# Optimization experiments

Hardware: AMD Instinct MI355X
Metric: run time of the kernel (lower is better)

## Reference

```python
import jax, jax.numpy as jnp
import numpy as np

LN_EPS = 1e-5  # torch nn.LayerNorm default
L2_EPS = 1e-12  # F.normalize default


def layer_norm(x, gamma, beta):
    mu = jnp.mean(x, axis=-1, keepdims=True)
    var = jnp.mean(jnp.square(x - mu), axis=-1, keepdims=True)
    return (x - mu) * jax.lax.rsqrt(var + LN_EPS) * gamma + beta


def l2_normalize(x):
    n = jnp.linalg.norm(x, axis=-1, keepdims=True)
    return x / jnp.maximum(n, L2_EPS)


def setup_inputs() -> dict:
    key = jax.random.key(0)
    k_x, k_mu = jax.random.split(key, 2)
    B, C, H, W = 4, 512, 128, 128
    K, M = 19, 5  # num_classes, num_components_per_class
    x = jax.random.normal(k_x, (B, C, H, W), dtype=jnp.float32)
    means = 0.02 * jax.random.normal(k_mu, (K, M, C), dtype=jnp.float32)  # trunc_normal_(std=0.02)
    diagonal = jnp.ones((K, M, C), dtype=jnp.float32)
    feat_gamma = jnp.ones((C,), dtype=jnp.float32)
    feat_beta = jnp.zeros((C,), dtype=jnp.float32)
    mask_gamma = jnp.ones((K,), dtype=jnp.float32)
    mask_beta = jnp.zeros((K,), dtype=jnp.float32)
    return dict(x=x, means=means, diagonal=diagonal,
                feat_gamma=feat_gamma, feat_beta=feat_beta,
                mask_gamma=mask_gamma, mask_beta=mask_beta)


def reference(x, means, diagonal, feat_gamma, feat_beta, mask_gamma, mask_beta):
    B, C, H, W = x.shape
    K, M, D = means.shape
    # rearrange 'b c h w -> (b h w) c'
    f = jnp.transpose(x, (0, 2, 3, 1)).reshape(-1, C)  # (N, D)
    f = layer_norm(f, feat_gamma, feat_beta)
    f = l2_normalize(f)
    # means are re-normalized in-place each forward
    mu = l2_normalize(means).reshape(K * M, D)          # (P, D), P = K*M
    sigma = diagonal.reshape(K * M, D)                  # diagonal scale (std)
    inv_var = 1.0 / jnp.square(sigma)
    # Mahalanobis distance via quadratic expansion (avoids (N,P,D) intermediate):
    # sum_d ((f - mu)/sigma)^2 = f^2 . iv - 2 f . (mu*iv) + sum(mu^2 * iv)
    q1 = jnp.square(f) @ inv_var.T                      # (N, P)
    q2 = f @ (mu * inv_var).T                           # (N, P)
    q3 = jnp.sum(jnp.square(mu) * inv_var, axis=-1)     # (P,)
    maha = q1 - 2.0 * q2 + q3[None, :]
    log_det = jnp.sum(jnp.log(sigma), axis=-1)          # sum log sigma, (P,)
    half_log2pi = 0.5 * D * jnp.log(2.0 * jnp.pi)
    log_prob = -0.5 * maha - log_det[None, :] - half_log2pi  # (N, P)
    log_prob = log_prob.reshape(-1, K, M)
    m_prob = jnp.max(log_prob, axis=-1)                 # amax over components, (N, K)
    out = layer_norm(m_prob, mask_gamma, mask_beta)
    # rearrange '(b h w) k -> b k h w'
    out_seg = jnp.transpose(out.reshape(B, H, W, K), (0, 3, 1, 2))
    return out_seg
```

## Files before the change

kernel.cpp:

```cpp
#include <hip/hip_runtime.h>
#include <math.h>

#define C_ 512
#define HW_ 16384
#define K_ 19
#define M_ 5
#define P_ 95
#define P2 96
#define TPX 32
#define NBLK 2048
#define HL2PI 470.49652900081467f

typedef __attribute__((ext_vector_type(8))) short short8;
typedef __attribute__((ext_vector_type(4))) float float4v;

static __device__ __forceinline__ short f2bf(float f) {
  unsigned u = __builtin_bit_cast(unsigned, f);
  unsigned r = (u + 0x7fffu + ((u >> 16) & 1u)) >> 16;
  return (short)r;
}

__device__ __forceinline__ float block_reduce_sum(float v, volatile float* red) {
#pragma unroll
  for (int o = 32; o; o >>= 1) v += __shfl_down(v, o);
  const int lane = threadIdx.x & 63, wv = threadIdx.x >> 6;
  if (lane == 0) red[wv] = v;
  __syncthreads();
  float r = red[0] + red[1] + red[2] + red[3];
  __syncthreads();
  return r;
}

__global__ __launch_bounds__(256) void prep_kernel(
    const float* __restrict__ means, const float* __restrict__ diag,
    short* __restrict__ wbf, float* __restrict__ cterm) {
  const int p = blockIdx.x;
  const int tid = threadIdx.x;
  __shared__ float red[4];
  if (p >= P_) {
    for (int c = tid; c < C_; c += 256) {
      wbf[p * 1024 + c] = 0;
      wbf[p * 1024 + 512 + c] = 0;
    }
    if (tid == 0) cterm[p] = 0.f;
    return;
  }
  const float* mrow = means + (size_t)p * C_;
  const float* srow = diag + (size_t)p * C_;
  float m0 = mrow[tid], m1 = mrow[tid + 256];
  float ss = block_reduce_sum(m0 * m0 + m1 * m1, red);
  float rden = 1.f / fmaxf(sqrtf(ss), 1e-12f);
  float q3 = 0.f, ld = 0.f;
#pragma unroll
  for (int t = 0; t < 2; t++) {
    int c = tid + t * 256;
    float m = mrow[c], s = srow[c];
    float mu = m * rden;
    float iv = 1.f / (s * s);
    wbf[p * 1024 + c] = f2bf(iv);
    wbf[p * 1024 + 512 + c] = f2bf(mu * iv);
    q3 += mu * mu * iv;
    ld += logf(s);
  }
  q3 = block_reduce_sum(q3, red);
  ld = block_reduce_sum(ld, red);
  if (tid == 0) cterm[p] = -0.5f * q3 - ld - HL2PI;
}

__global__ __launch_bounds__(256) void main_kernel(
    const float* __restrict__ x,
    const float* __restrict__ fg, const float* __restrict__ fb,
    const float* __restrict__ mg, const float* __restrict__ mb,
    const short* __restrict__ wbf, const float* __restrict__ cterm,
    float* __restrict__ out) {
  __shared__ __align__(16) char raw[65536];
  __shared__ float red0[8 * TPX], red1[8 * TPX];
  __shared__ float meanA[TPX], rstdA[TPX], rnA[TPX], rn2A[TPX];
  __shared__ float mean2A[TPX], rstd2A[TPX];
  __shared__ float mpr[TPX * 20];

  const int tid = threadIdx.x;
  const int px = tid & 31, part = tid >> 5;
  const int n0 = blockIdx.x * TPX;
  const int b = n0 >> 14;
  const int rem = n0 & 16383;
  const int h = rem >> 7;
  const int w0 = rem & 127;

  const float* xp = x + (size_t)b * C_ * HW_ + h * 128 + w0 + px;
  const int cbase = part * 64;
  float xr[64];
#pragma unroll
  for (int i = 0; i < 64; i++) xr[i] = xp[(size_t)(cbase + i) * HW_];
  {
    float s = 0.f, q = 0.f;
#pragma unroll
    for (int i = 0; i < 64; i++) {
      s += xr[i];
      q += xr[i] * xr[i];
    }
    red0[part * 32 + px] = s;
    red1[part * 32 + px] = q;
  }
  __syncthreads();
  if (tid < 32) {
    float ss = 0.f, qq = 0.f;
#pragma unroll
    for (int i = 0; i < 8; i++) {
      ss += red0[i * 32 + tid];
      qq += red1[i * 32 + tid];
    }
    float mean = ss * (1.f / C_);
    float var = qq * (1.f / C_) - mean * mean;
    meanA[tid] = mean;
    rstdA[tid] = rsqrtf(var + 1e-5f);
  }
  __syncthreads();

  {
    const float mean = meanA[px], rstd = rstdA[px];
    float s2 = 0.f;
    const int t_ = px >> 4;
    const int lq = px & 15;
#pragma unroll
    for (int t8 = 0; t8 < 8; t8++) {
      const int c0 = cbase + t8 * 8;
      short8 v2p, vp;
#pragma unroll
      for (int j = 0; j < 8; j++) {
        const int c = c0 + j;
        float v = (xr[t8 * 8 + j] - mean) * rstd;
        v = fmaf(v, fg[c], fb[c]);
        s2 += v * v;
        v2p[j] = f2bf(v * v);
        vp[j] = f2bf(v);
      }
      const int l = (((c0 >> 3) & 3) << 4) | lq;
      const int ks1 = c0 >> 5;
      const int ks2 = 16 + ks1;
      *(short8*)(raw + (((t_ * 32 + ks1) << 10) | (l << 4))) = v2p;
      *(short8*)(raw + (((t_ * 32 + ks2) << 10) | (l << 4))) = vp;
    }
    red0[part * 32 + px] = s2;
  }
  __syncthreads();
  if (tid < 32) {
    float ss = 0.f;
#pragma unroll
    for (int i = 0; i < 8; i++) ss += red0[i * 32 + tid];
    float rn = 1.f / fmaxf(sqrtf(ss), 1e-12f);
    rnA[tid] = rn;
    rn2A[tid] = rn * rn;
  }
  __syncthreads();

  const int wv = tid >> 6, lane = tid & 63;
  const int pbase = (wv & 1) * 3;
  const int khalf = wv >> 1;
  const int lm = lane & 15, lk = lane >> 4;
  float4v acc[3][2] = {};
  const short* wrow = wbf + (((pbase * 16 + lm) << 10) | (khalf << 9) | (lk << 3));
#pragma unroll 4
  for (int ksl = 0; ksl < 16; ksl++) {
    const int ks = khalf * 16 + ksl;
    short8 a0 = *(const short8*)(wrow + ksl * 32);
    short8 a1 = *(const short8*)(wrow + 16384 + ksl * 32);
    short8 a2 = *(const short8*)(wrow + 32768 + ksl * 32);
    short8 b0 = *(const short8*)(raw + ((ks << 10) | (lane << 4)));
    short8 b1 = *(const short8*)(raw + (((32 + ks) << 10) | (lane << 4)));
    acc[0][0] = __builtin_amdgcn_mfma_f32_16x16x32_bf16(a0, b0, acc[0][0], 0, 0, 0);
    acc[0][1] = __builtin_amdgcn_mfma_f32_16x16x32_bf16(a0, b1, acc[0][1], 0, 0, 0);
    acc[1][0] = __builtin_amdgcn_mfma_f32_16x16x32_bf16(a1, b0, acc[1][0], 0, 0, 0);
    acc[1][1] = __builtin_amdgcn_mfma_f32_16x16x32_bf16(a1, b1, acc[1][1], 0, 0, 0);
    acc[2][0] = __builtin_amdgcn_mfma_f32_16x16x32_bf16(a2, b0, acc[2][0], 0, 0, 0);
    acc[2][1] = __builtin_amdgcn_mfma_f32_16x16x32_bf16(a2, b1, acc[2][1], 0, 0, 0);
  }
  __syncthreads();
  float* lp = (float*)raw;

  if (khalf == 0) {
#pragma unroll
    for (int i = 0; i < 3; i++) {
      const int prow = (pbase + i) * 16 + lk * 4;
#pragma unroll
      for (int r = 0; r < 4; r++) {
        const float ct = cterm[prow + r];
#pragma unroll
        for (int t = 0; t < 2; t++) {
          const int pxx = t * 16 + lm;
          lp[pxx * 100 + prow + r] = fmaf(-0.5f * rn2A[pxx], acc[i][t][r], ct);
        }
      }
    }
  }
  __syncthreads();
  if (khalf == 1) {
#pragma unroll
    for (int i = 0; i < 3; i++) {
      const int prow = (pbase + i) * 16 + lk * 4;
#pragma unroll
      for (int r = 0; r < 4; r++) {
#pragma unroll
        for (int t = 0; t < 2; t++) {
          const int pxx = t * 16 + lm;
          lp[pxx * 100 + prow + r] += rnA[pxx] * acc[i][t][r];
        }
      }
    }
  }
  __syncthreads();

  for (int idx = tid; idx < TPX * K_; idx += 256) {
    const int pxx = idx / K_;
    const int k = idx - pxx * K_;
    const float* row = lp + pxx * 100 + k * M_;
    float mv = row[0];
#pragma unroll
    for (int m = 1; m < M_; m++) mv = fmaxf(mv, row[m]);
    mpr[pxx * 20 + k] = mv;
  }
  __syncthreads();
  if (tid < 32) {
    float ss = 0.f;
    for (int k = 0; k < K_; k++) ss += mpr[tid * 20 + k];
    float m2 = ss * (1.f / K_);
    float qq = 0.f;
    for (int k = 0; k < K_; k++) {
      float d = mpr[tid * 20 + k] - m2;
      qq += d * d;
    }
    mean2A[tid] = m2;
    rstd2A[tid] = rsqrtf(qq * (1.f / K_) + 1e-5f);
  }
  __syncthreads();
  float* obase = out + ((size_t)(b * K_) * 128 + h) * 128 + w0;
  for (int idx = tid; idx < TPX * K_; idx += 256) {
    const int k = idx >> 5, pxx = idx & 31;
    float v = fmaf((mpr[pxx * 20 + k] - mean2A[pxx]) * rstd2A[pxx], mg[k], mb[k]);
    obase[(size_t)k * HW_ + pxx] = v;
  }
}

extern "C" void kernel_launch(void* const* d_in, const int* in_sizes, int n_in,
                              void* d_out, int out_size, void* d_ws, size_t ws_size,
                              hipStream_t stream) {
  const float* x = (const float*)d_in[0];
  const float* means = (const float*)d_in[1];
  const float* diag = (const float*)d_in[2];
  const float* fg = (const float*)d_in[3];
  const float* fb = (const float*)d_in[4];
  const float* mg = (const float*)d_in[5];
  const float* mb = (const float*)d_in[6];
  float* out = (float*)d_out;

  short* wbf = (short*)d_ws;
  float* cterm = (float*)((char*)d_ws + (size_t)P2 * 1024 * 2);

  prep_kernel<<<P2, 256, 0, stream>>>(means, diag, wbf, cterm);
  main_kernel<<<NBLK, 256, 0, stream>>>(x, fg, fb, mg, mb, wbf, cterm, out);
}
```

Measured before the change: 81.45 us.

## Halve pixels per block, swizzle LDS layout, split partial-sum buffers

```diff
diff --git a/kernel.cpp b/kernel.cpp
--- a/kernel.cpp
+++ b/kernel.cpp
@@ -7,8 +7,8 @@
 #define M_ 5
 #define P_ 95
 #define P2 96
-#define TPX 32
-#define NBLK 2048
+#define TPX 16
+#define NBLK 4096
 #define HL2PI 470.49652900081467f
 
 typedef __attribute__((ext_vector_type(8))) short short8;
@@ -73,14 +73,16 @@
     const float* __restrict__ mg, const float* __restrict__ mb,
     const short* __restrict__ wbf, const float* __restrict__ cterm,
     float* __restrict__ out) {
-  __shared__ __align__(16) char raw[65536];
-  __shared__ float red0[8 * TPX], red1[8 * TPX];
+  __shared__ __align__(16) char raw[32768];
+  __shared__ float red0[4 * TPX], red1[4 * TPX];
   __shared__ float meanA[TPX], rstdA[TPX], rnA[TPX], rn2A[TPX];
   __shared__ float mean2A[TPX], rstd2A[TPX];
   __shared__ float mpr[TPX * 20];
 
   const int tid = threadIdx.x;
-  const int px = tid & 31, part = tid >> 5;
+  const int px = tid & 15;
+  const int part = tid >> 4;
+  const int wv = tid >> 6, lane = tid & 63;
   const int n0 = blockIdx.x * TPX;
   const int b = n0 >> 14;
   const int rem = n0 & 16383;
@@ -88,28 +90,26 @@
   const int w0 = rem & 127;
 
   const float* xp = x + (size_t)b * C_ * HW_ + h * 128 + w0 + px;
-  const int cbase = part * 64;
-  float xr[64];
-#pragma unroll
-  for (int i = 0; i < 64; i++) xr[i] = xp[(size_t)(cbase + i) * HW_];
+  const int cbase = part * 32;
+  float xr[32];
+#pragma unroll
+  for (int i = 0; i < 32; i++) xr[i] = xp[(size_t)(cbase + i) * HW_];
   {
     float s = 0.f, q = 0.f;
 #pragma unroll
-    for (int i = 0; i < 64; i++) {
+    for (int i = 0; i < 32; i++) {
       s += xr[i];
       q += xr[i] * xr[i];
     }
-    red0[part * 32 + px] = s;
-    red1[part * 32 + px] = q;
-  }
-  __syncthreads();
-  if (tid < 32) {
+    s += __shfl_xor(s, 16); s += __shfl_xor(s, 32);
+    q += __shfl_xor(q, 16); q += __shfl_xor(q, 32);
+    if (lane < 16) { red0[wv * 16 + px] = s; red1[wv * 16 + px] = q; }
+  }
+  __syncthreads();
+  if (tid < 16) {
     float ss = 0.f, qq = 0.f;
 #pragma unroll
-    for (int i = 0; i < 8; i++) {
-      ss += red0[i * 32 + tid];
-      qq += red1[i * 32 + tid];
-    }
+    for (int i = 0; i < 4; i++) { ss += red0[i * 16 + tid]; qq += red1[i * 16 + tid]; }
     float mean = ss * (1.f / C_);
     float var = qq * (1.f / C_) - mean * mean;
     meanA[tid] = mean;
@@ -120,10 +120,9 @@
   {
     const float mean = meanA[px], rstd = rstdA[px];
     float s2 = 0.f;
-    const int t_ = px >> 4;
-    const int lq = px & 15;
-#pragma unroll
-    for (int t8 = 0; t8 < 8; t8++) {
+    const int swz = (part & 3) << 8;
+#pragma unroll
+    for (int t8 = 0; t8 < 4; t8++) {
       const int c0 = cbase + t8 * 8;
       short8 v2p, vp;
 #pragma unroll
@@ -135,77 +134,59 @@
         v2p[j] = f2bf(v * v);
         vp[j] = f2bf(v);
       }
-      const int l = (((c0 >> 3) & 3) << 4) | lq;
-      const int ks1 = c0 >> 5;
-      const int ks2 = 16 + ks1;
-      *(short8*)(raw + (((t_ * 32 + ks1) << 10) | (l << 4))) = v2p;
-      *(short8*)(raw + (((t_ * 32 + ks2) << 10) | (l << 4))) = vp;
-    }
-    red0[part * 32 + px] = s2;
-  }
-  __syncthreads();
-  if (tid < 32) {
+      const int a1 = ((part << 10) | (t8 << 8) | (px << 4)) ^ swz;
+      *(short8*)(raw + a1) = v2p;
+      *(short8*)(raw + a1 + 16384) = vp;
+    }
+    s2 += __shfl_xor(s2, 16); s2 += __shfl_xor(s2, 32);
+    if (lane < 16) red0[wv * 16 + px] = s2;
+  }
+  __syncthreads();
+  if (tid < 16) {
     float ss = 0.f;
 #pragma unroll
-    for (int i = 0; i < 8; i++) ss += red0[i * 32 + tid];
+    for (int i = 0; i < 4; i++) ss += red0[i * 16 + tid];
     float rn = 1.f / fmaxf(sqrtf(ss), 1e-12f);
     rnA[tid] = rn;
     rn2A[tid] = rn * rn;
   }
   __syncthreads();
 
-  const int wv = tid >> 6, lane = tid & 63;
   const int pbase = (wv & 1) * 3;
   const int khalf = wv >> 1;
   const int lm = lane & 15, lk = lane >> 4;
-  float4v acc[3][2] = {};
-  const short* wrow = wbf + (((pbase * 16 + lm) << 10) | (khalf << 9) | (lk << 3));
+  float4v acc[3] = {};
+  const short* wrow = wbf + (((pbase * 16 + lm) << 10) + (khalf << 9) + (lk << 3));
 #pragma unroll 4
   for (int ksl = 0; ksl < 16; ksl++) {
     const int ks = khalf * 16 + ksl;
     short8 a0 = *(const short8*)(wrow + ksl * 32);
     short8 a1 = *(const short8*)(wrow + 16384 + ksl * 32);
     short8 a2 = *(const short8*)(wrow + 32768 + ksl * 32);
-    short8 b0 = *(const short8*)(raw + ((ks << 10) | (lane << 4)));
-    short8 b1 = *(const short8*)(raw + (((32 + ks) << 10) | (lane << 4)));
-    acc[0][0] = __builtin_amdgcn_mfma_f32_16x16x32_bf16(a0, b0, acc[0][0], 0, 0, 0);
-    acc[0][1] = __builtin_amdgcn_mfma_f32_16x16x32_bf16(a0, b1, acc[0][1], 0, 0, 0);
-    acc[1][0] = __builtin_amdgcn_mfma_f32_16x16x32_bf16(a1, b0, acc[1][0], 0, 0, 0);
-    acc[1][1] = __builtin_amdgcn_mfma_f32_16x16x32_bf16(a1, b1, acc[1][1], 0, 0, 0);
-    acc[2][0] = __builtin_amdgcn_mfma_f32_16x16x32_bf16(a2, b0, acc[2][0], 0, 0, 0);
-    acc[2][1] = __builtin_amdgcn_mfma_f32_16x16x32_bf16(a2, b1, acc[2][1], 0, 0, 0);
-  }
-  __syncthreads();
-  float* lp = (float*)raw;
+    short8 bf = *(const short8*)(raw + (((ks << 10) | (lane << 4)) ^ ((ks & 3) << 8)));
+    acc[0] = __builtin_amdgcn_mfma_f32_16x16x32_bf16(a0, bf, acc[0], 0, 0, 0);
+    acc[1] = __builtin_amdgcn_mfma_f32_16x16x32_bf16(a1, bf, acc[1], 0, 0, 0);
+    acc[2] = __builtin_amdgcn_mfma_f32_16x16x32_bf16(a2, bf, acc[2], 0, 0, 0);
+  }
+  __syncthreads();
+  float* lp1 = (float*)raw;
+  float* lp2 = (float*)(raw + 8192);
 
   if (khalf == 0) {
 #pragma unroll
     for (int i = 0; i < 3; i++) {
       const int prow = (pbase + i) * 16 + lk * 4;
 #pragma unroll
-      for (int r = 0; r < 4; r++) {
-        const float ct = cterm[prow + r];
-#pragma unroll
-        for (int t = 0; t < 2; t++) {
-          const int pxx = t * 16 + lm;
-          lp[pxx * 100 + prow + r] = fmaf(-0.5f * rn2A[pxx], acc[i][t][r], ct);
-        }
-      }
-    }
-  }
-  __syncthreads();
-  if (khalf == 1) {
+      for (int r = 0; r < 4; r++)
+        lp1[lm * 96 + prow + r] = fmaf(-0.5f * rn2A[lm], acc[i][r], cterm[prow + r]);
+    }
+  } else {
 #pragma unroll
     for (int i = 0; i < 3; i++) {
       const int prow = (pbase + i) * 16 + lk * 4;
 #pragma unroll
-      for (int r = 0; r < 4; r++) {
-#pragma unroll
-        for (int t = 0; t < 2; t++) {
-          const int pxx = t * 16 + lm;
-          lp[pxx * 100 + prow + r] += rnA[pxx] * acc[i][t][r];
-        }
-      }
+      for (int r = 0; r < 4; r++)
+        lp2[lm * 96 + prow + r] = rnA[lm] * acc[i][r];
     }
   }
   __syncthreads();
@@ -213,14 +194,15 @@
   for (int idx = tid; idx < TPX * K_; idx += 256) {
     const int pxx = idx / K_;
     const int k = idx - pxx * K_;
-    const float* row = lp + pxx * 100 + k * M_;
-    float mv = row[0];
-#pragma unroll
-    for (int m = 1; m < M_; m++) mv = fmaxf(mv, row[m]);
+    const float* r1 = lp1 + pxx * 96 + k * M_;
+    const float* r2 = lp2 + pxx * 96 + k * M_;
+    float mv = r1[0] + r2[0];
+#pragma unroll
+    for (int m = 1; m < M_; m++) mv = fmaxf(mv, r1[m] + r2[m]);
     mpr[pxx * 20 + k] = mv;
   }
   __syncthreads();
-  if (tid < 32) {
+  if (tid < 16) {
     float ss = 0.f;
     for (int k = 0; k < K_; k++) ss += mpr[tid * 20 + k];
     float m2 = ss * (1.f / K_);
@@ -235,7 +217,7 @@
   __syncthreads();
   float* obase = out + ((size_t)(b * K_) * 128 + h) * 128 + w0;
   for (int idx = tid; idx < TPX * K_; idx += 256) {
-    const int k = idx >> 5, pxx = idx & 31;
+    const int k = idx >> 4, pxx = idx & 15;
     float v = fmaf((mpr[pxx * 20 + k] - mean2A[pxx]) * rstd2A[pxx], mg[k], mb[k]);
     obase[(size_t)k * HW_ + pxx] = v;
   }
```

Measured after the change: 126.2 us. +55.0%, slower.

## Make main kernel persistent with 4 tiles per block and prefetch next tile's input

Applied to the files above, without the earlier changes.

```diff
diff --git a/kernel.cpp b/kernel.cpp
--- a/kernel.cpp
+++ b/kernel.cpp
@@ -8,7 +8,8 @@
 #define P_ 95
 #define P2 96
 #define TPX 32
-#define NBLK 2048
+#define GRID_ 512
+#define TILES_ 4
 #define HL2PI 470.49652900081467f
 
 typedef __attribute__((ext_vector_type(8))) short short8;
@@ -78,166 +79,188 @@
   __shared__ float meanA[TPX], rstdA[TPX], rnA[TPX], rn2A[TPX];
   __shared__ float mean2A[TPX], rstd2A[TPX];
   __shared__ float mpr[TPX * 20];
+  __shared__ float fgs[C_], fbs[C_], cts[P2], mgs[K_ + 1], mbs[K_ + 1];
 
   const int tid = threadIdx.x;
   const int px = tid & 31, part = tid >> 5;
-  const int n0 = blockIdx.x * TPX;
-  const int b = n0 >> 14;
-  const int rem = n0 & 16383;
-  const int h = rem >> 7;
-  const int w0 = rem & 127;
-
-  const float* xp = x + (size_t)b * C_ * HW_ + h * 128 + w0 + px;
-  const int cbase = part * 64;
-  float xr[64];
-#pragma unroll
-  for (int i = 0; i < 64; i++) xr[i] = xp[(size_t)(cbase + i) * HW_];
-  {
-    float s = 0.f, q = 0.f;
-#pragma unroll
-    for (int i = 0; i < 64; i++) {
-      s += xr[i];
-      q += xr[i] * xr[i];
-    }
-    red0[part * 32 + px] = s;
-    red1[part * 32 + px] = q;
-  }
-  __syncthreads();
-  if (tid < 32) {
-    float ss = 0.f, qq = 0.f;
-#pragma unroll
-    for (int i = 0; i < 8; i++) {
-      ss += red0[i * 32 + tid];
-      qq += red1[i * 32 + tid];
-    }
-    float mean = ss * (1.f / C_);
-    float var = qq * (1.f / C_) - mean * mean;
-    meanA[tid] = mean;
-    rstdA[tid] = rsqrtf(var + 1e-5f);
-  }
-  __syncthreads();
-
-  {
-    const float mean = meanA[px], rstd = rstdA[px];
-    float s2 = 0.f;
-    const int t_ = px >> 4;
-    const int lq = px & 15;
-#pragma unroll
-    for (int t8 = 0; t8 < 8; t8++) {
-      const int c0 = cbase + t8 * 8;
-      short8 v2p, vp;
-#pragma unroll
-      for (int j = 0; j < 8; j++) {
-        const int c = c0 + j;
-        float v = (xr[t8 * 8 + j] - mean) * rstd;
-        v = fmaf(v, fg[c], fb[c]);
-        s2 += v * v;
-        v2p[j] = f2bf(v * v);
-        vp[j] = f2bf(v);
-      }
-      const int l = (((c0 >> 3) & 3) << 4) | lq;
-      const int ks1 = c0 >> 5;
-      const int ks2 = 16 + ks1;
-      *(short8*)(raw + (((t_ * 32 + ks1) << 10) | (l << 4))) = v2p;
-      *(short8*)(raw + (((t_ * 32 + ks2) << 10) | (l << 4))) = vp;
-    }
-    red0[part * 32 + px] = s2;
-  }
-  __syncthreads();
-  if (tid < 32) {
-    float ss = 0.f;
-#pragma unroll
-    for (int i = 0; i < 8; i++) ss += red0[i * 32 + tid];
-    float rn = 1.f / fmaxf(sqrtf(ss), 1e-12f);
-    rnA[tid] = rn;
-    rn2A[tid] = rn * rn;
-  }
-  __syncthreads();
-
   const int wv = tid >> 6, lane = tid & 63;
   const int pbase = (wv & 1) * 3;
   const int khalf = wv >> 1;
   const int lm = lane & 15, lk = lane >> 4;
-  float4v acc[3][2] = {};
-  const short* wrow = wbf + (((pbase * 16 + lm) << 10) | (khalf << 9) | (lk << 3));
+  const int cbase = part * 64;
+
+  for (int i = tid; i < C_; i += 256) { fgs[i] = fg[i]; fbs[i] = fb[i]; }
+  if (tid < P2) cts[tid] = cterm[tid];
+  if (tid < K_) { mgs[tid] = mg[tid]; mbs[tid] = mb[tid]; }
+
+  float xr[64];
+  {
+    const int n0 = blockIdx.x * TPX;
+    const int b = n0 >> 14, rem = n0 & 16383, h = rem >> 7, w0 = rem & 127;
+    const float* xp = x + (size_t)b * C_ * HW_ + h * 128 + w0 + px;
+#pragma unroll
+    for (int i = 0; i < 64; i++) xr[i] = xp[(size_t)(cbase + i) * HW_];
+  }
+
+  for (int t = 0; t < TILES_; ++t) {
+    const int n0 = (blockIdx.x + GRID_ * t) * TPX;
+    const int b = n0 >> 14, rem = n0 & 16383, h = rem >> 7, w0 = rem & 127;
+
+    {
+      float s = 0.f, q = 0.f;
+#pragma unroll
+      for (int i = 0; i < 64; i++) {
+        s += xr[i];
+        q += xr[i] * xr[i];
+      }
+      red0[part * 32 + px] = s;
+      red1[part * 32 + px] = q;
+    }
+    __syncthreads();
+    if (tid < 32) {
+      float ss = 0.f, qq = 0.f;
+#pragma unroll
+      for (int i = 0; i < 8; i++) {
+        ss += red0[i * 32 + tid];
+        qq += red1[i * 32 + tid];
+      }
+      float mean = ss * (1.f / C_);
+      float var = qq * (1.f / C_) - mean * mean;
+      meanA[tid] = mean;
+      rstdA[tid] = rsqrtf(var + 1e-5f);
+    }
+    __syncthreads();
+
+    {
+      const float mean = meanA[px], rstd = rstdA[px];
+      float s2 = 0.f;
+      const int t_ = px >> 4;
+      const int lq = px & 15;
+#pragma unroll
+      for (int t8 = 0; t8 < 8; t8++) {
+        const int c0 = cbase + t8 * 8;
+        short8 v2p, vp;
+#pragma unroll
+        for (int j = 0; j < 8; j++) {
+          const int c = c0 + j;
+          float v = (xr[t8 * 8 + j] - mean) * rstd;
+          v = fmaf(v, fgs[c], fbs[c]);
+          s2 += v * v;
+          v2p[j] = f2bf(v * v);
+          vp[j] = f2bf(v);
+        }
+        const int l = (((c0 >> 3) & 3) << 4) | lq;
+        const int ks1 = c0 >> 5;
+        const int ks2 = 16 + ks1;
+        *(short8*)(raw + (((t_ * 32 + ks1) << 10) | (l << 4))) = v2p;
+        *(short8*)(raw + (((t_ * 32 + ks2) << 10) | (l << 4))) = vp;
+      }
+      red0[part * 32 + px] = s2;
+    }
+    __syncthreads();
+    if (tid < 32) {
+      float ss = 0.f;
+#pragma unroll
+      for (int i = 0; i < 8; i++) ss += red0[i * 32 + tid];
+      float rn = 1.f / fmaxf(sqrtf(ss), 1e-12f);
+      rnA[tid] = rn;
+      rn2A[tid] = rn * rn;
+    }
+    __syncthreads();
+
+    float4v acc[3][2] = {{}, {}, {}};
+    const short* wrow = wbf + (((pbase * 16 + lm) << 10) + (khalf << 9) + (lk << 3));
 #pragma unroll 4
-  for (int ksl = 0; ksl < 16; ksl++) {
-    const int ks = khalf * 16 + ksl;
-    short8 a0 = *(const short8*)(wrow + ksl * 32);
-    short8 a1 = *(const short8*)(wrow + 16384 + ksl * 32);
-    short8 a2 = *(const short8*)(wrow + 32768 + ksl * 32);
-    short8 b0 = *(const short8*)(raw + ((ks << 10) | (lane << 4)));
-    short8 b1 = *(const short8*)(raw + (((32 + ks) << 10) | (lane << 4)));
-    acc[0][0] = __builtin_amdgcn_mfma_f32_16x16x32_bf16(a0, b0, acc[0][0], 0, 0, 0);
-    acc[0][1] = __builtin_amdgcn_mfma_f32_16x16x32_bf16(a0, b1, acc[0][1], 0, 0, 0);
-    acc[1][0] = __builtin_amdgcn_mfma_f32_16x16x32_bf16(a1, b0, acc[1][0], 0, 0, 0);
-    acc[1][1] = __builtin_amdgcn_mfma_f32_16x16x32_bf16(a1, b1, acc[1][1], 0, 0, 0);
-    acc[2][0] = __builtin_amdgcn_mfma_f32_16x16x32_bf16(a2, b0, acc[2][0], 0, 0, 0);
-    acc[2][1] = __builtin_amdgcn_mfma_f32_16x16x32_bf16(a2, b1, acc[2][1], 0, 0, 0);
-  }
-  __syncthreads();
-  float* lp = (float*)raw;
-
-  if (khalf == 0) {
-#pragma unroll
-    for (int i = 0; i < 3; i++) {
-      const int prow = (pbase + i) * 16 + lk * 4;
-#pragma unroll
-      for (int r = 0; r < 4; r++) {
-        const float ct = cterm[prow + r];
-#pragma unroll
-        for (int t = 0; t < 2; t++) {
-          const int pxx = t * 16 + lm;
-          lp[pxx * 100 + prow + r] = fmaf(-0.5f * rn2A[pxx], acc[i][t][r], ct);
+    for (int ksl = 0; ksl < 16; ksl++) {
+      const int ks = khalf * 16 + ksl;
+      short8 a0 = *(const short8*)(wrow + ksl * 32);
+      short8 a1 = *(const short8*)(wrow + 16384 + ksl * 32);
+      short8 a2 = *(const short8*)(wrow + 32768 + ksl * 32);
+      short8 b0 = *(const short8*)(raw + ((ks << 10) | (lane << 4)));
+      short8 b1 = *(const short8*)(raw + (((32 + ks) << 10) | (lane << 4)));
+      acc[0][0] = __builtin_amdgcn_mfma_f32_16x16x32_bf16(a0, b0, acc[0][0], 0, 0, 0);
+      acc[0][1] = __builtin_amdgcn_mfma_f32_16x16x32_bf16(a0, b1, acc[0][1], 0, 0, 0);
+      acc[1][0] = __builtin_amdgcn_mfma_f32_16x16x32_bf16(a1, b0, acc[1][0], 0, 0, 0);
+      acc[1][1] = __builtin_amdgcn_mfma_f32_16x16x32_bf16(a1, b1, acc[1][1], 0, 0, 0);
+      acc[2][0] = __builtin_amdgcn_mfma_f32_16x16x32_bf16(a2, b0, acc[2][0], 0, 0, 0);
+      acc[2][1] = __builtin_amdgcn_mfma_f32_16x16x32_bf16(a2, b1, acc[2][1], 0, 0, 0);
+    }
+
+    __builtin_amdgcn_sched_barrier(0);
+    if (t + 1 < TILES_) {
+      const int n0n = (blockIdx.x + GRID_ * (t + 1)) * TPX;
+      const int bn = n0n >> 14, remn = n0n & 16383, hn = remn >> 7, w0n = remn & 127;
+      const float* xpn = x + (size_t)bn * C_ * HW_ + hn * 128 + w0n + px;
+#pragma unroll
+      for (int i = 0; i < 64; i++) xr[i] = xpn[(size_t)(cbase + i) * HW_];
+    }
+    __builtin_amdgcn_sched_barrier(0);
+
+    __syncthreads();
+    float* lp = (float*)raw;
+
+    if (khalf == 0) {
+#pragma unroll
+      for (int i = 0; i < 3; i++) {
+        const int prow = (pbase + i) * 16 + lk * 4;
+#pragma unroll
+        for (int r = 0; r < 4; r++) {
+          const float ct = cts[prow + r];
+#pragma unroll
+          for (int t2 = 0; t2 < 2; t2++) {
+            const int pxx = t2 * 16 + lm;
+            lp[pxx * 100 + prow + r] = fmaf(-0.5f * rn2A[pxx], acc[i][t2][r], ct);
+          }
         }
       }
     }
-  }
-  __syncthreads();
-  if (khalf == 1) {
-#pragma unroll
-    for (int i = 0; i < 3; i++) {
-      const int prow = (pbase + i) * 16 + lk * 4;
-#pragma unroll
-      for (int r = 0; r < 4; r++) {
-#pragma unroll
-        for (int t = 0; t < 2; t++) {
-          const int pxx = t * 16 + lm;
-          lp[pxx * 100 + prow + r] += rnA[pxx] * acc[i][t][r];
+    __syncthreads();
+    if (khalf == 1) {
+#pragma unroll
+      for (int i = 0; i < 3; i++) {
+        const int prow = (pbase + i) * 16 + lk * 4;
+#pragma unroll
+        for (int r = 0; r < 4; r++) {
+#pragma unroll
+          for (int t2 = 0; t2 < 2; t2++) {
+            const int pxx = t2 * 16 + lm;
+            lp[pxx * 100 + prow + r] += rnA[pxx] * acc[i][t2][r];
+          }
         }
       }
     }
-  }
-  __syncthreads();
-
-  for (int idx = tid; idx < TPX * K_; idx += 256) {
-    const int pxx = idx / K_;
-    const int k = idx - pxx * K_;
-    const float* row = lp + pxx * 100 + k * M_;
-    float mv = row[0];
-#pragma unroll
-    for (int m = 1; m < M_; m++) mv = fmaxf(mv, row[m]);
-    mpr[pxx * 20 + k] = mv;
-  }
-  __syncthreads();
-  if (tid < 32) {
-    float ss = 0.f;
-    for (int k = 0; k < K_; k++) ss += mpr[tid * 20 + k];
-    float m2 = ss * (1.f / K_);
-    float qq = 0.f;
-    for (int k = 0; k < K_; k++) {
-      float d = mpr[tid * 20 + k] - m2;
-      qq += d * d;
-    }
-    mean2A[tid] = m2;
-    rstd2A[tid] = rsqrtf(qq * (1.f / K_) + 1e-5f);
-  }
-  __syncthreads();
-  float* obase = out + ((size_t)(b * K_) * 128 + h) * 128 + w0;
-  for (int idx = tid; idx < TPX * K_; idx += 256) {
-    const int k = idx >> 5, pxx = idx & 31;
-    float v = fmaf((mpr[pxx * 20 + k] - mean2A[pxx]) * rstd2A[pxx], mg[k], mb[k]);
-    obase[(size_t)k * HW_ + pxx] = v;
+    __syncthreads();
+
+    for (int idx = tid; idx < TPX * K_; idx += 256) {
+      const int pxx = idx / K_;
+      const int k = idx - pxx * K_;
+      const float* row = lp + pxx * 100 + k * M_;
+      float mv = row[0];
+#pragma unroll
+      for (int m = 1; m < M_; m++) mv = fmaxf(mv, row[m]);
+      mpr[pxx * 20 + k] = mv;
+    }
+    __syncthreads();
+    if (tid < 32) {
+      float ss = 0.f;
+      for (int k = 0; k < K_; k++) ss += mpr[tid * 20 + k];
+      float m2 = ss * (1.f / K_);
+      float qq = 0.f;
+      for (int k = 0; k < K_; k++) {
+        float d = mpr[tid * 20 + k] - m2;
+        qq += d * d;
+      }
+      mean2A[tid] = m2;
+      rstd2A[tid] = rsqrtf(qq * (1.f / K_) + 1e-5f);
+    }
+    __syncthreads();
+    float* obase = out + ((size_t)(b * K_) * 128 + h) * 128 + w0;
+    for (int idx = tid; idx < TPX * K_; idx += 256) {
+      const int k = idx >> 5, pxx = idx & 31;
+      float v = fmaf((mpr[pxx * 20 + k] - mean2A[pxx]) * rstd2A[pxx], mgs[k], mbs[k]);
+      obase[(size_t)k * HW_ + pxx] = v;
+    }
+    __syncthreads();
   }
 }
 
@@ -257,5 +280,5 @@
   float* cterm = (float*)((char*)d_ws + (size_t)P2 * 1024 * 2);
 
   prep_kernel<<<P2, 256, 0, stream>>>(means, diag, wbf, cterm);
-  main_kernel<<<NBLK, 256, 0, stream>>>(x, fg, fb, mg, mb, wbf, cterm, out);
-}
+  main_kernel<<<GRID_, 256, 0, stream>>>(x, fg, fb, mg, mb, wbf, cterm, out);
+}
```

Result: slower. 97.41 us (+19.6%).

## Halve LDS tile, drop x register cache, square bf16 operands on the fly

Applied to the files above, without the earlier changes.

```diff
diff --git a/kernel.cpp b/kernel.cpp
--- a/kernel.cpp
+++ b/kernel.cpp
@@ -18,6 +18,16 @@
   unsigned u = __builtin_bit_cast(unsigned, f);
   unsigned r = (u + 0x7fffu + ((u >> 16) & 1u)) >> 16;
   return (short)r;
+}
+
+static __device__ __forceinline__ short8 sq8(short8 a) {
+  short8 r;
+#pragma unroll
+  for (int j = 0; j < 8; j++) {
+    float f = __builtin_bit_cast(float, ((unsigned)(unsigned short)a[j]) << 16);
+    r[j] = f2bf(f * f);
+  }
+  return r;
 }
 
 __device__ __forceinline__ float block_reduce_sum(float v, volatile float* red) {
@@ -73,7 +83,7 @@
     const float* __restrict__ mg, const float* __restrict__ mb,
     const short* __restrict__ wbf, const float* __restrict__ cterm,
     float* __restrict__ out) {
-  __shared__ __align__(16) char raw[65536];
+  __shared__ __align__(16) char raw[32768];
   __shared__ float red0[8 * TPX], red1[8 * TPX];
   __shared__ float meanA[TPX], rstdA[TPX], rnA[TPX], rn2A[TPX];
   __shared__ float mean2A[TPX], rstd2A[TPX];
@@ -81,23 +91,27 @@
 
   const int tid = threadIdx.x;
   const int px = tid & 31, part = tid >> 5;
+  const int wv = tid >> 6, lane = tid & 63;
   const int n0 = blockIdx.x * TPX;
   const int b = n0 >> 14;
   const int rem = n0 & 16383;
   const int h = rem >> 7;
   const int w0 = rem & 127;
-
+  const int cbase = part * 64;
   const float* xp = x + (size_t)b * C_ * HW_ + h * 128 + w0 + px;
-  const int cbase = part * 64;
-  float xr[64];
-#pragma unroll
-  for (int i = 0; i < 64; i++) xr[i] = xp[(size_t)(cbase + i) * HW_];
+
   {
     float s = 0.f, q = 0.f;
-#pragma unroll
-    for (int i = 0; i < 64; i++) {
-      s += xr[i];
-      q += xr[i] * xr[i];
+#pragma unroll 1
+    for (int t16 = 0; t16 < 4; t16++) {
+      float xv[16];
+#pragma unroll
+      for (int i = 0; i < 16; i++) xv[i] = xp[(size_t)(cbase + t16 * 16 + i) * HW_];
+#pragma unroll
+      for (int i = 0; i < 16; i++) {
+        s += xv[i];
+        q += xv[i] * xv[i];
+      }
     }
     red0[part * 32 + px] = s;
     red1[part * 32 + px] = q;
@@ -122,24 +136,20 @@
     float s2 = 0.f;
     const int t_ = px >> 4;
     const int lq = px & 15;
-#pragma unroll
+#pragma unroll 2
     for (int t8 = 0; t8 < 8; t8++) {
       const int c0 = cbase + t8 * 8;
-      short8 v2p, vp;
+      float xv[8];
+#pragma unroll
+      for (int j = 0; j < 8; j++) xv[j] = xp[(size_t)(c0 + j) * HW_];
+      short8 vp;
 #pragma unroll
       for (int j = 0; j < 8; j++) {
-        const int c = c0 + j;
-        float v = (xr[t8 * 8 + j] - mean) * rstd;
-        v = fmaf(v, fg[c], fb[c]);
+        float v = fmaf((xv[j] - mean) * rstd, fg[c0 + j], fb[c0 + j]);
         s2 += v * v;
-        v2p[j] = f2bf(v * v);
         vp[j] = f2bf(v);
       }
-      const int l = (((c0 >> 3) & 3) << 4) | lq;
-      const int ks1 = c0 >> 5;
-      const int ks2 = 16 + ks1;
-      *(short8*)(raw + (((t_ * 32 + ks1) << 10) | (l << 4))) = v2p;
-      *(short8*)(raw + (((t_ * 32 + ks2) << 10) | (l << 4))) = vp;
+      *(short8*)(raw + (((t_ * 16 + (c0 >> 5)) << 10) | (((c0 >> 3) & 3) << 8) | (lq << 4))) = vp;
     }
     red0[part * 32 + px] = s2;
   }
@@ -154,20 +164,22 @@
   }
   __syncthreads();
 
-  const int wv = tid >> 6, lane = tid & 63;
   const int pbase = (wv & 1) * 3;
   const int khalf = wv >> 1;
   const int lm = lane & 15, lk = lane >> 4;
-  float4v acc[3][2] = {};
-  const short* wrow = wbf + (((pbase * 16 + lm) << 10) | (khalf << 9) | (lk << 3));
+  float4v acc[3][2] = {{}, {}, {}};
+  const short* wrow = wbf + (((pbase * 16 + lm) << 10) + (khalf << 9) + (lk << 3));
 #pragma unroll 4
   for (int ksl = 0; ksl < 16; ksl++) {
-    const int ks = khalf * 16 + ksl;
     short8 a0 = *(const short8*)(wrow + ksl * 32);
     short8 a1 = *(const short8*)(wrow + 16384 + ksl * 32);
     short8 a2 = *(const short8*)(wrow + 32768 + ksl * 32);
-    short8 b0 = *(const short8*)(raw + ((ks << 10) | (lane << 4)));
-    short8 b1 = *(const short8*)(raw + (((32 + ks) << 10) | (lane << 4)));
+    short8 b0 = *(const short8*)(raw + ((ksl << 10) | (lane << 4)));
+    short8 b1 = *(const short8*)(raw + (((16 + ksl) << 10) | (lane << 4)));
+    if (khalf == 0) {
+      b0 = sq8(b0);
+      b1 = sq8(b1);
+    }
     acc[0][0] = __builtin_amdgcn_mfma_f32_16x16x32_bf16(a0, b0, acc[0][0], 0, 0, 0);
     acc[0][1] = __builtin_amdgcn_mfma_f32_16x16x32_bf16(a0, b1, acc[0][1], 0, 0, 0);
     acc[1][0] = __builtin_amdgcn_mfma_f32_16x16x32_bf16(a1, b0, acc[1][0], 0, 0, 0);
@@ -186,9 +198,9 @@
       for (int r = 0; r < 4; r++) {
         const float ct = cterm[prow + r];
 #pragma unroll
-        for (int t = 0; t < 2; t++) {
-          const int pxx = t * 16 + lm;
-          lp[pxx * 100 + prow + r] = fmaf(-0.5f * rn2A[pxx], acc[i][t][r], ct);
+        for (int t2 = 0; t2 < 2; t2++) {
+          const int pxx = t2 * 16 + lm;
+          lp[pxx * 100 + prow + r] = fmaf(-0.5f * rn2A[pxx], acc[i][t2][r], ct);
         }
       }
     }
@@ -201,9 +213,9 @@
 #pragma unroll
       for (int r = 0; r < 4; r++) {
 #pragma unroll
-        for (int t = 0; t < 2; t++) {
-          const int pxx = t * 16 + lm;
-          lp[pxx * 100 + prow + r] += rnA[pxx] * acc[i][t][r];
+        for (int t2 = 0; t2 < 2; t2++) {
+          const int pxx = t2 * 16 + lm;
+          lp[pxx * 100 + prow + r] += rnA[pxx] * acc[i][t2][r];
         }
       }
     }
```

Result: no change. 81.63 us (+0.2%).
